# Performance work log

Hardware: AMD Instinct MI355X
Metric: run time of the kernel (lower is better)

The kernel has to match this reference:

```python
import jax, jax.numpy as jnp
import numpy as np
import math

S, B, H, NH = 2048, 1, 4096, 32
D = H // NH  # 128 head dim


def rotate_half(x):
    x1, x2 = x[..., : x.shape[-1] // 2], x[..., x.shape[-1] // 2 :]
    return jnp.concatenate((-x2, x1), axis=-1)


def setup_inputs() -> dict:
    key = jax.random.key(0)
    k1, k2, k3, k4, k5 = jax.random.split(key, 5)
    hidden_states = jax.random.normal(k1, (S, B, H), dtype=jnp.float32)
    position_ids = jnp.broadcast_to(jnp.arange(S, dtype=jnp.int32)[None, :], (B, S))
    # causal mask: True = masked (upper triangle above diagonal)
    attention_mask = jnp.triu(jnp.ones((S, S), dtype=bool), k=1)[None, None]
    W_qkv = jax.random.normal(k2, (H, 3 * H), dtype=jnp.float32) * 0.02
    b_qkv = jax.random.normal(k3, (3 * H,), dtype=jnp.float32) * 0.02
    W_dense = jax.random.normal(k4, (H, H), dtype=jnp.float32) * 0.02
    b_dense = jax.random.normal(k5, (H,), dtype=jnp.float32) * 0.02
    return {
        "hidden_states": hidden_states,
        "position_ids": position_ids,
        "attention_mask": attention_mask,
        "W_qkv": W_qkv,
        "b_qkv": b_qkv,
        "W_dense": W_dense,
        "b_dense": b_dense,
        "layer_id": 27,
    }


def reference(hidden_states, position_ids, attention_mask, W_qkv, b_qkv, W_dense, b_dense, layer_id):
    s, b, h = hidden_states.shape
    nh, d = NH, D
    # QKV projection: [s, b, 3h] -> [s, b, nh, 3d] -> split
    mixed = hidden_states @ W_qkv + b_qkv
    mixed = mixed.reshape(s, b, nh, 3 * d)
    q, k, v = jnp.split(mixed, 3, axis=-1)  # each [s, b, nh, d]
    # rotary embedding indexed by position_ids (transposed to [s, b])
    pos = position_ids.T  # [s, b]
    inv_freq = 1.0 / (10000.0 ** (jnp.arange(0, d, 2, dtype=jnp.float32) / d))
    freqs = pos[..., None].astype(jnp.float32) * inv_freq  # [s, b, d/2]
    emb = jnp.concatenate((freqs, freqs), axis=-1)  # [s, b, d]
    cos = jnp.cos(emb)[:, :, None, :]  # [s, b, 1, d]
    sin = jnp.sin(emb)[:, :, None, :]
    q = q * cos + rotate_half(q) * sin
    k = k * cos + rotate_half(k) * sin
    # attention with per-layer scaling coeff (cancels in softmax except mask fill)
    coeff = jnp.float32(layer_id + 1)
    q_scaled = q / (math.sqrt(d) * coeff)
    scores = jnp.einsum("sbnd,tbnd->bnst", q_scaled, k)  # [b, nh, s, s]
    scores = jnp.where(attention_mask, jnp.float32(-10000.0), scores) * coeff
    probs = jax.nn.softmax(scores, axis=-1)
    ctx = jnp.einsum("bnst,tbnd->sbnd", probs, v).reshape(s, b, h)
    out = ctx @ W_dense + b_dense
    return out
```

## Files before the change

kernel.cpp:

```cpp
#include <hip/hip_runtime.h>

#define S_LEN 2048
#define HID   4096
#define NHEAD 32
#define DHEAD 128
#define H3    12288

typedef __attribute__((ext_vector_type(8))) __bf16 bf16x8;
typedef __attribute__((ext_vector_type(4))) __bf16 bf16x4;
typedef __attribute__((ext_vector_type(4))) float  f32x4;

__device__ __forceinline__ void gl_lds16(const void* g, void* l) {
  __builtin_amdgcn_global_load_lds(
      (const __attribute__((address_space(1))) void*)g,
      (__attribute__((address_space(3))) void*)l, 16, 0, 0);
}

__global__ void cvt_f32_bf16(const float* __restrict__ in, __bf16* __restrict__ out, int n4) {
  int i = blockIdx.x * blockDim.x + threadIdx.x;
  if (i >= n4) return;
  float4 v = ((const float4*)in)[i];
  bf16x4 o;
  o.x = (__bf16)v.x; o.y = (__bf16)v.y; o.z = (__bf16)v.z; o.w = (__bf16)v.w;
  ((bf16x4*)out)[i] = o;
}

__global__ void transpose_cvt(const float* __restrict__ in, __bf16* __restrict__ out, int R, int C) {
  __shared__ float t[64][65];
  const int tid = threadIdx.x;
  const int r0 = blockIdx.y * 64, c0 = blockIdx.x * 64;
#pragma unroll
  for (int p = 0; p < 4; ++p) {
    int r = p * 16 + (tid >> 4);
    int c4 = (tid & 15) * 4;
    float4 v = *(const float4*)(in + (size_t)(r0 + r) * C + c0 + c4);
    t[r][c4] = v.x; t[r][c4 + 1] = v.y; t[r][c4 + 2] = v.z; t[r][c4 + 3] = v.w;
  }
  __syncthreads();
#pragma unroll
  for (int p = 0; p < 4; ++p) {
    int c = p * 16 + (tid >> 4);
    int rg = (tid & 15) * 4;
    bf16x4 o;
    o.x = (__bf16)t[rg][c]; o.y = (__bf16)t[rg + 1][c];
    o.z = (__bf16)t[rg + 2][c]; o.w = (__bf16)t[rg + 3][c];
    *(bf16x4*)(out + (size_t)(c0 + c) * R + r0 + rg) = o;
  }
}

__global__ void rope_kernel(__bf16* __restrict__ q, __bf16* __restrict__ k,
                            const int* __restrict__ pos) {
  int idx = blockIdx.x * 256 + threadIdx.x;
  int j = idx & 63;
  int hs = idx >> 6;
  int s = hs & (S_LEN - 1);
  float p = (float)pos[s];
  float invf = __expf(-(float)j * (9.210340371976184f / 64.f));
  float a = p * invf;
  float c, sn;
  __sincosf(a, &sn, &c);
  const float SC = 0.08838834764831845f;
  size_t base = (size_t)hs * 128;
  float x1 = (float)q[base + j], x2 = (float)q[base + j + 64];
  q[base + j]      = (__bf16)((x1 * c - x2 * sn) * SC);
  q[base + j + 64] = (__bf16)((x2 * c + x1 * sn) * SC);
  x1 = (float)k[base + j]; x2 = (float)k[base + j + 64];
  k[base + j]      = (__bf16)(x1 * c - x2 * sn);
  k[base + j + 64] = (__bf16)(x2 * c + x1 * sn);
}

template <int EPI>
__global__ __launch_bounds__(256, 2)
void gemm_db(const __bf16* __restrict__ A, const __bf16* __restrict__ BT,
             const float* __restrict__ bias, int K,
             __bf16* __restrict__ outq, __bf16* __restrict__ outk,
             __bf16* __restrict__ outvt, float* __restrict__ outf) {
  const int tid = threadIdx.x;
  const int lane = tid & 63;
  const int wave = tid >> 6;
  const int nwg = gridDim.x;
  const int q8 = nwg >> 3;
  const int flat = blockIdx.x;
  const int swz = (flat & 7) * q8 + (flat >> 3);
  const int bm = (swz & 15) * 128;
  const int bn = (swz >> 4) * 128;

  __shared__ char lds[2][32768];

  f32x4 acc[4][4] = {};

  const int wm = (wave >> 1) * 64;
  const int wn = (wave & 1) * 64;

  const int sr = tid >> 3;
  const int sc = (tid & 7) * 16;
  const int scs = sc ^ ((sr & 7) << 4);

  const char* Arow = (const char*)(A + (size_t)(bm + sr) * K) + scs;
  const char* Brow = (const char*)(BT + (size_t)(bn + sr) * K) + scs;

  const int NT = K >> 6;

  auto stage = [&](int t) {
    const char* a_src = Arow + (size_t)t * 128;
    const char* b_src = Brow + (size_t)t * 128;
    char* a_dst = lds[t & 1] + wave * 1024;
    char* b_dst = lds[t & 1] + 16384 + wave * 1024;
#pragma unroll
    for (int i = 0; i < 4; ++i) {
      gl_lds16(a_src + (size_t)i * 32 * K * 2, a_dst + i * 4096);
      gl_lds16(b_src + (size_t)i * 32 * K * 2, b_dst + i * 4096);
    }
  };

  stage(0);
  __syncthreads();
  for (int t = 0; t < NT; ++t) {
    if (t + 1 < NT) stage(t + 1);
    const char* Ab = lds[t & 1];
    const char* Bb = lds[t & 1] + 16384;
#pragma unroll
    for (int kk = 0; kk < 2; ++kk) {
      bf16x8 af[4], bfr[4];
#pragma unroll
      for (int m = 0; m < 4; ++m) {
        int row = wm + m * 16 + (lane & 15);
        int cb = (kk * 64 + ((lane >> 4) << 4)) ^ ((row & 7) << 4);
        af[m] = *(const bf16x8*)(Ab + row * 128 + cb);
      }
#pragma unroll
      for (int n = 0; n < 4; ++n) {
        int row = wn + n * 16 + (lane & 15);
        int cb = (kk * 64 + ((lane >> 4) << 4)) ^ ((row & 7) << 4);
        bfr[n] = *(const bf16x8*)(Bb + row * 128 + cb);
      }
#pragma unroll
      for (int m = 0; m < 4; ++m)
#pragma unroll
        for (int n = 0; n < 4; ++n)
          acc[m][n] = __builtin_amdgcn_mfma_f32_16x16x32_bf16(af[m], bfr[n], acc[m][n], 0, 0, 0);
    }
    __syncthreads();
  }

  const int rbase = (lane >> 4) << 2;
  const int cl = lane & 15;
  if (EPI == 0) {
    const int route = (bn >> 7) % 3;
    const int head = bn / 384;
#pragma unroll
    for (int n = 0; n < 4; ++n) {
      const int d = wn + n * 16 + cl;
      const float bv = bias[bn + d];
#pragma unroll
      for (int m = 0; m < 4; ++m) {
        const int srow = bm + wm + m * 16 + rbase;
        if (route == 2) {
          bf16x4 o;
          o.x = (__bf16)(acc[m][n][0] + bv);
          o.y = (__bf16)(acc[m][n][1] + bv);
          o.z = (__bf16)(acc[m][n][2] + bv);
          o.w = (__bf16)(acc[m][n][3] + bv);
          *(bf16x4*)(outvt + ((size_t)head * 128 + d) * S_LEN + srow) = o;
        } else {
          __bf16* dst = (route == 0 ? outq : outk) + (size_t)head * S_LEN * 128;
#pragma unroll
          for (int r = 0; r < 4; ++r)
            dst[(size_t)(srow + r) * 128 + d] = (__bf16)(acc[m][n][r] + bv);
        }
      }
    }
  } else {
#pragma unroll
    for (int n = 0; n < 4; ++n) {
      const int col = bn + wn + n * 16 + cl;
      const float bv = bias[col];
#pragma unroll
      for (int m = 0; m < 4; ++m) {
        const int srow = bm + wm + m * 16 + rbase;
#pragma unroll
        for (int r = 0; r < 4; ++r)
          outf[(size_t)(srow + r) * HID + col] = acc[m][n][r] + bv;
      }
    }
  }
}

#define ATTN_PROCESS(QF, OACC, MROW, LROW, QT)                                  \
  {                                                                             \
    f32x4 sacc[4] = {};                                                         \
    _Pragma("unroll")                                                           \
    for (int kk = 0; kk < 4; ++kk) {                                            \
      bf16x8 bk[4];                                                             \
      _Pragma("unroll")                                                         \
      for (int n = 0; n < 4; ++n) {                                             \
        int row = n * 16 + cl;                                                  \
        int cb = (kk * 64 + ((lane >> 4) << 4)) ^ ((row & 7) << 4);             \
        bk[n] = *(const bf16x8*)(Kb + row * 256 + cb);                          \
      }                                                                         \
      _Pragma("unroll")                                                         \
      for (int n = 0; n < 4; ++n)                                               \
        sacc[n] = __builtin_amdgcn_mfma_f32_16x16x32_bf16(QF[kk], bk[n], sacc[n], 0, 0, 0); \
    }                                                                           \
    float pmax[4];                                                              \
    _Pragma("unroll")                                                           \
    for (int r = 0; r < 4; ++r) pmax[r] = -1e30f;                               \
    if (j == (QT)) {                                                            \
      _Pragma("unroll")                                                         \
      for (int n = 0; n < 4; ++n) {                                             \
        const int col = n * 16 + cl;                                            \
        _Pragma("unroll")                                                       \
        for (int r = 0; r < 4; ++r) {                                           \
          const int row = wave * 16 + rbase + r;                                \
          float sv = (col > row) ? -1e30f : sacc[n][r];                         \
          sacc[n][r] = sv;                                                      \
          pmax[r] = fmaxf(pmax[r], sv);                                         \
        }                                                                       \
      }                                                                         \
    } else {                                                                    \
      _Pragma("unroll")                                                         \
      for (int n = 0; n < 4; ++n)                                               \
        _Pragma("unroll")                                                       \
        for (int r = 0; r < 4; ++r)                                             \
          pmax[r] = fmaxf(pmax[r], sacc[n][r]);                                 \
    }                                                                           \
    _Pragma("unroll")                                                           \
    for (int xm = 1; xm < 16; xm <<= 1)                                         \
      _Pragma("unroll")                                                         \
      for (int r = 0; r < 4; ++r)                                               \
        pmax[r] = fmaxf(pmax[r], __shfl_xor(pmax[r], xm, 64));                  \
    const bool okd = (pmax[0] <= MROW[0] + 8.f) && (pmax[1] <= MROW[1] + 8.f) && \
                     (pmax[2] <= MROW[2] + 8.f) && (pmax[3] <= MROW[3] + 8.f);  \
    if (__all(okd)) {                                                           \
      _Pragma("unroll")                                                         \
      for (int r = 0; r < 4; ++r) {                                             \
        float psum = 0.f;                                                       \
        _Pragma("unroll")                                                       \
        for (int n = 0; n < 4; ++n) {                                           \
          float pe = __expf(sacc[n][r] - MROW[r]);                              \
          sacc[n][r] = pe;                                                      \
          psum += pe;                                                           \
        }                                                                       \
        _Pragma("unroll")                                                       \
        for (int xm = 1; xm < 16; xm <<= 1)                                     \
          psum += __shfl_xor(psum, xm, 64);                                     \
        LROW[r] += psum;                                                        \
      }                                                                         \
    } else {                                                                    \
      _Pragma("unroll")                                                         \
      for (int r = 0; r < 4; ++r) {                                             \
        const float mnew = fmaxf(MROW[r], pmax[r]);                             \
        const float alpha = __expf(MROW[r] - mnew);                             \
        MROW[r] = mnew;                                                         \
        float psum = 0.f;                                                       \
        _Pragma("unroll")                                                       \
        for (int n = 0; n < 4; ++n) {                                           \
          float pe = __expf(sacc[n][r] - mnew);                                 \
          sacc[n][r] = pe;                                                      \
          psum += pe;                                                           \
        }                                                                       \
        _Pragma("unroll")                                                       \
        for (int xm = 1; xm < 16; xm <<= 1)                                     \
          psum += __shfl_xor(psum, xm, 64);                                     \
        LROW[r] = LROW[r] * alpha + psum;                                       \
        _Pragma("unroll")                                                       \
        for (int nd = 0; nd < 8; ++nd)                                          \
          OACC[nd][r] *= alpha;                                                 \
      }                                                                         \
    }                                                                           \
    _Pragma("unroll")                                                           \
    for (int n = 0; n < 4; ++n) {                                               \
      const int colb = (n * 16 + cl) * 2;                                       \
      _Pragma("unroll")                                                         \
      for (int r = 0; r < 4; ++r) {                                             \
        const int row = rbase + r;                                              \
        *(__bf16*)(Pb + row * 128 + (colb ^ ((row & 7) << 4))) = (__bf16)sacc[n][r]; \
      }                                                                         \
    }                                                                           \
    _Pragma("unroll")                                                           \
    for (int kk = 0; kk < 2; ++kk) {                                            \
      bf16x8 pa, bv[8];                                                         \
      {                                                                         \
        int row = cl;                                                           \
        int cb = (kk * 64 + ((lane >> 4) << 4)) ^ ((row & 7) << 4);             \
        pa = *(const bf16x8*)(Pb + row * 128 + cb);                             \
      }                                                                         \
      _Pragma("unroll")                                                         \
      for (int nd = 0; nd < 8; ++nd) {                                          \
        int row = nd * 16 + cl;                                                 \
        int cb = (kk * 64 + ((lane >> 4) << 4)) ^ ((row & 7) << 4);             \
        bv[nd] = *(const bf16x8*)(Vb + row * 128 + cb);                         \
      }                                                                         \
      _Pragma("unroll")                                                         \
      for (int nd = 0; nd < 8; ++nd)                                            \
        OACC[nd] = __builtin_amdgcn_mfma_f32_16x16x32_bf16(pa, bv[nd], OACC[nd], 0, 0, 0); \
    }                                                                           \
  }

__global__ __launch_bounds__(256, 2)
void attn_kernel(const __bf16* __restrict__ q, const __bf16* __restrict__ k,
                 const __bf16* __restrict__ vt, __bf16* __restrict__ ctx) {
  const int flat = blockIdx.x;
  const int swz = (flat & 7) * 64 + (flat >> 3);
  const int p = swz & 15;
  const int h = swz >> 4;
  const int tid = threadIdx.x, lane = tid & 63, wave = tid >> 6;
  __shared__ char Kd[2][16384];
  __shared__ char Vd[2][16384];
  __shared__ __bf16 Ps[4][16 * 64];
  char* Pb = (char*)(Ps[wave]);

  const __bf16* qh = q + (size_t)h * S_LEN * 128;
  const __bf16* kh = k + (size_t)h * S_LEN * 128;
  const __bf16* vh = vt + (size_t)h * 128 * S_LEN;

  const int cl = lane & 15, rbase = (lane >> 4) << 2;

  const int krow = tid >> 4, kcol = (tid & 15) * 16;
  const int kcs = kcol ^ ((krow & 7) << 4);
  const int vrow = tid >> 3, vcol = (tid & 7) * 16;
  const int vcs = vcol ^ ((vrow & 7) << 4);

  auto stage_kv = [&](int j) {
    {
      const char* src = (const char*)(kh + (size_t)(j * 64 + krow) * 128) + kcs;
      char* dst = Kd[j & 1] + wave * 1024;
#pragma unroll
      for (int i = 0; i < 4; ++i)
        gl_lds16(src + (size_t)i * 16 * 256, dst + i * 4096);
    }
    {
      const char* src = (const char*)(vh + (size_t)vrow * S_LEN + j * 64) + vcs;
      char* dst = Vd[j & 1] + wave * 1024;
#pragma unroll
      for (int i = 0; i < 4; ++i)
        gl_lds16(src + (size_t)i * 32 * (S_LEN * 2), dst + i * 4096);
    }
  };

  const int qtA = p, qtB = 31 - p;

  bf16x8 qfA[4], qfB[4];
  {
    const int rA = qtA * 64 + wave * 16 + cl;
    const int rB = qtB * 64 + wave * 16 + cl;
#pragma unroll
    for (int kk = 0; kk < 4; ++kk) {
      qfA[kk] = *(const bf16x8*)(qh + (size_t)rA * 128 + kk * 32 + ((lane >> 4) << 3));
      qfB[kk] = *(const bf16x8*)(qh + (size_t)rB * 128 + kk * 32 + ((lane >> 4) << 3));
    }
  }

  f32x4 oA[8] = {}, oB[8] = {};
  float mA[4], lA[4], mB[4], lB[4];
#pragma unroll
  for (int r = 0; r < 4; ++r) { mA[r] = -1e30f; lA[r] = 0.f; mB[r] = -1e30f; lB[r] = 0.f; }

  stage_kv(0);
  __syncthreads();
  for (int j = 0; j <= qtB; ++j) {
    if (j < qtB) stage_kv(j + 1);
    const char* Kb = Kd[j & 1];
    const char* Vb = Vd[j & 1];
    ATTN_PROCESS(qfB, oB, mB, lB, qtB)
    if (j <= qtA) ATTN_PROCESS(qfA, oA, mA, lA, qtA)
    __syncthreads();
  }

#pragma unroll
  for (int nd = 0; nd < 8; ++nd) {
    const int d = nd * 16 + cl;
#pragma unroll
    for (int r = 0; r < 4; ++r) {
      const int srowA = qtA * 64 + wave * 16 + rbase + r;
      const int srowB = qtB * 64 + wave * 16 + rbase + r;
      ctx[(size_t)srowA * HID + h * 128 + d] = (__bf16)(oA[nd][r] / lA[r]);
      ctx[(size_t)srowB * HID + h * 128 + d] = (__bf16)(oB[nd][r] / lB[r]);
    }
  }
}

extern "C" void kernel_launch(void* const* d_in, const int* in_sizes, int n_in,
                              void* d_out, int out_size, void* d_ws, size_t ws_size,
                              hipStream_t stream) {
  const float* hs = (const float*)d_in[0];
  const int* pos = (const int*)d_in[1];
  const float* wqkv = (const float*)d_in[3];
  const float* bqkv = (const float*)d_in[4];
  const float* wd = (const float*)d_in[5];
  const float* bd = (const float*)d_in[6];
  float* out = (float*)d_out;

  char* ws = (char*)d_ws;
  const size_t MB = 1024ull * 1024ull;
  if (ws_size < 160 * MB) return;
  __bf16* wT  = (__bf16*)(ws);
  __bf16* xb  = (__bf16*)(ws + 96 * MB);
  __bf16* qb_ = (__bf16*)(ws + 112 * MB);
  __bf16* kb_ = (__bf16*)(ws + 128 * MB);
  __bf16* vtb = (__bf16*)(ws + 144 * MB);

  cvt_f32_bf16<<<8192, 256, 0, stream>>>(hs, xb, 2097152);
  transpose_cvt<<<dim3(192, 64), 256, 0, stream>>>(wqkv, wT, 4096, 12288);
  gemm_db<0><<<1536, 256, 0, stream>>>(xb, wT, bqkv, 4096, qb_, kb_, vtb, nullptr);
  rope_kernel<<<16384, 256, 0, stream>>>(qb_, kb_, pos);
  transpose_cvt<<<dim3(64, 64), 256, 0, stream>>>(wd, wT, 4096, 4096);
  attn_kernel<<<512, 256, 0, stream>>>(qb_, kb_, vtb, xb);
  gemm_db<1><<<512, 256, 0, stream>>>(xb, wT, bd, 4096, nullptr, nullptr, nullptr, out);
}
```

Before: 457.4 us.

## Add 8-wave triple-buffered QKV GEMM with split-K staging and MFMA priority hints

```diff
diff --git a/kernel.cpp b/kernel.cpp
--- a/kernel.cpp
+++ b/kernel.cpp
@@ -69,19 +69,15 @@
   k[base + j + 64] = (__bf16)(x2 * c + x1 * sn);
 }
 
-template <int EPI>
 __global__ __launch_bounds__(256, 2)
-void gemm_db(const __bf16* __restrict__ A, const __bf16* __restrict__ BT,
-             const float* __restrict__ bias, int K,
-             __bf16* __restrict__ outq, __bf16* __restrict__ outk,
-             __bf16* __restrict__ outvt, float* __restrict__ outf) {
+void gemm_dense(const __bf16* __restrict__ A, const __bf16* __restrict__ BT,
+                const float* __restrict__ bias, int K,
+                float* __restrict__ outf) {
   const int tid = threadIdx.x;
   const int lane = tid & 63;
   const int wave = tid >> 6;
-  const int nwg = gridDim.x;
-  const int q8 = nwg >> 3;
   const int flat = blockIdx.x;
-  const int swz = (flat & 7) * q8 + (flat >> 3);
+  const int swz = (flat & 7) * 64 + (flat >> 3);
   const int bm = (swz & 15) * 128;
   const int bn = (swz >> 4) * 128;
 
@@ -145,42 +141,145 @@
 
   const int rbase = (lane >> 4) << 2;
   const int cl = lane & 15;
-  if (EPI == 0) {
-    const int route = (bn >> 7) % 3;
-    const int head = bn / 384;
-#pragma unroll
-    for (int n = 0; n < 4; ++n) {
-      const int d = wn + n * 16 + cl;
-      const float bv = bias[bn + d];
+#pragma unroll
+  for (int n = 0; n < 4; ++n) {
+    const int col = bn + wn + n * 16 + cl;
+    const float bv = bias[col];
+#pragma unroll
+    for (int m = 0; m < 4; ++m) {
+      const int srow = bm + wm + m * 16 + rbase;
+#pragma unroll
+      for (int r = 0; r < 4; ++r)
+        outf[(size_t)(srow + r) * HID + col] = acc[m][n][r] + bv;
+    }
+  }
+}
+
+__global__ __launch_bounds__(512, 2)
+void gemm8p(const __bf16* __restrict__ A, const __bf16* __restrict__ BT,
+            const float* __restrict__ bias, int K,
+            __bf16* __restrict__ outq, __bf16* __restrict__ outk,
+            __bf16* __restrict__ outvt) {
+  const int tid = threadIdx.x, lane = tid & 63, wave = tid >> 6;
+  const int flat = blockIdx.x;
+  const int swz = (flat & 7) * 96 + (flat >> 3);
+  const int bm = (swz & 7) * 256;
+  const int bn = (swz >> 3) * 128;
+
+  __shared__ char lds[3 * 49152];
+
+  const int widM = wave >> 1, widN = wave & 1;
+  const int cl = lane & 15;
+  const int hi16 = (lane >> 4) << 4;
+  const int rbase = (lane >> 4) << 2;
+
+  const int K2 = K * 2;
+  const int sr = tid >> 3;
+  const int scs = ((tid & 7) * 16) ^ ((sr & 7) << 4);
+  const char* Asrc = (const char*)A + (size_t)(bm + sr) * K2 + scs;
+  const char* Bsrc = (const char*)BT + (size_t)(bn + sr) * K2 + scs;
+
+  f32x4 acc[4][4] = {};
+  const int NT = K >> 6;
+
+  auto stageA = [&](int t) {
+    char* d = lds + (t % 3) * 49152 + wave * 1024;
+    const char* s = Asrc + (size_t)t * 128;
+#pragma unroll
+    for (int i = 0; i < 4; ++i)
+      gl_lds16(s + (size_t)(i * 64) * K2, d + i * 8192);
+  };
+  auto stageB = [&](int t) {
+    char* d = lds + (t % 3) * 49152 + 32768 + wave * 1024;
+    const char* s = Bsrc + (size_t)t * 128;
+#pragma unroll
+    for (int i = 0; i < 2; ++i)
+      gl_lds16(s + (size_t)(i * 64) * K2, d + i * 8192);
+  };
+
+  stageA(0); stageB(0); stageA(1); stageB(1);
+  asm volatile("s_waitcnt vmcnt(6)" ::: "memory");
+  asm volatile("s_barrier" ::: "memory");
+
+  for (int t = 0; t < NT; ++t) {
+    const char* sA = lds + (t % 3) * 49152;
+    const char* sB = sA + 32768;
+    {
+      bf16x8 af[4], bfr[4];
 #pragma unroll
       for (int m = 0; m < 4; ++m) {
-        const int srow = bm + wm + m * 16 + rbase;
-        if (route == 2) {
-          bf16x4 o;
-          o.x = (__bf16)(acc[m][n][0] + bv);
-          o.y = (__bf16)(acc[m][n][1] + bv);
-          o.z = (__bf16)(acc[m][n][2] + bv);
-          o.w = (__bf16)(acc[m][n][3] + bv);
-          *(bf16x4*)(outvt + ((size_t)head * 128 + d) * S_LEN + srow) = o;
-        } else {
-          __bf16* dst = (route == 0 ? outq : outk) + (size_t)head * S_LEN * 128;
-#pragma unroll
-          for (int r = 0; r < 4; ++r)
-            dst[(size_t)(srow + r) * 128 + d] = (__bf16)(acc[m][n][r] + bv);
-        }
-      }
-    }
-  } else {
-#pragma unroll
-    for (int n = 0; n < 4; ++n) {
-      const int col = bn + wn + n * 16 + cl;
-      const float bv = bias[col];
+        const int row = widM * 64 + m * 16 + cl;
+        af[m] = *(const bf16x8*)(sA + row * 128 + (hi16 ^ ((row & 7) << 4)));
+      }
+#pragma unroll
+      for (int n = 0; n < 4; ++n) {
+        const int row = widN * 64 + n * 16 + cl;
+        bfr[n] = *(const bf16x8*)(sB + row * 128 + (hi16 ^ ((row & 7) << 4)));
+      }
+      if (t + 2 < NT) stageA(t + 2);
+      asm volatile("s_barrier" ::: "memory");
+      asm volatile("s_waitcnt lgkmcnt(0)" ::: "memory");
+      __builtin_amdgcn_s_setprio(1);
+#pragma unroll
+      for (int m = 0; m < 4; ++m)
+#pragma unroll
+        for (int n = 0; n < 4; ++n)
+          acc[m][n] = __builtin_amdgcn_mfma_f32_16x16x32_bf16(af[m], bfr[n], acc[m][n], 0, 0, 0);
+      __builtin_amdgcn_s_setprio(0);
+      asm volatile("s_barrier" ::: "memory");
+    }
+    {
+      bf16x8 af[4], bfr[4];
 #pragma unroll
       for (int m = 0; m < 4; ++m) {
-        const int srow = bm + wm + m * 16 + rbase;
+        const int row = widM * 64 + m * 16 + cl;
+        af[m] = *(const bf16x8*)(sA + row * 128 + ((64 + hi16) ^ ((row & 7) << 4)));
+      }
+#pragma unroll
+      for (int n = 0; n < 4; ++n) {
+        const int row = widN * 64 + n * 16 + cl;
+        bfr[n] = *(const bf16x8*)(sB + row * 128 + ((64 + hi16) ^ ((row & 7) << 4)));
+      }
+      if (t + 2 < NT) {
+        stageB(t + 2);
+        asm volatile("s_waitcnt vmcnt(6)" ::: "memory");
+      } else {
+        asm volatile("s_waitcnt vmcnt(0)" ::: "memory");
+      }
+      asm volatile("s_barrier" ::: "memory");
+      asm volatile("s_waitcnt lgkmcnt(0)" ::: "memory");
+      __builtin_amdgcn_s_setprio(1);
+#pragma unroll
+      for (int m = 0; m < 4; ++m)
+#pragma unroll
+        for (int n = 0; n < 4; ++n)
+          acc[m][n] = __builtin_amdgcn_mfma_f32_16x16x32_bf16(af[m], bfr[n], acc[m][n], 0, 0, 0);
+      __builtin_amdgcn_s_setprio(0);
+      asm volatile("s_barrier" ::: "memory");
+    }
+  }
+
+  const int route = (bn >> 7) % 3;
+  const int head = bn / 384;
+#pragma unroll
+  for (int n = 0; n < 4; ++n) {
+    const int d = widN * 64 + n * 16 + cl;
+    const float bv = bias[bn + d];
+#pragma unroll
+    for (int m = 0; m < 4; ++m) {
+      const int srow = bm + widM * 64 + m * 16 + rbase;
+      if (route == 2) {
+        bf16x4 o;
+        o.x = (__bf16)(acc[m][n][0] + bv);
+        o.y = (__bf16)(acc[m][n][1] + bv);
+        o.z = (__bf16)(acc[m][n][2] + bv);
+        o.w = (__bf16)(acc[m][n][3] + bv);
+        *(bf16x4*)(outvt + ((size_t)head * 128 + d) * S_LEN + srow) = o;
+      } else {
+        __bf16* dst = (route == 0 ? outq : outk) + (size_t)head * S_LEN * 128;
 #pragma unroll
         for (int r = 0; r < 4; ++r)
-          outf[(size_t)(srow + r) * HID + col] = acc[m][n][r] + bv;
+          dst[(size_t)(srow + r) * 128 + d] = (__bf16)(acc[m][n][r] + bv);
       }
     }
   }
@@ -198,9 +297,11 @@
         int cb = (kk * 64 + ((lane >> 4) << 4)) ^ ((row & 7) << 4);             \
         bk[n] = *(const bf16x8*)(Kb + row * 256 + cb);                          \
       }                                                                         \
+      __builtin_amdgcn_s_setprio(1);                                            \
       _Pragma("unroll")                                                         \
       for (int n = 0; n < 4; ++n)                                               \
         sacc[n] = __builtin_amdgcn_mfma_f32_16x16x32_bf16(QF[kk], bk[n], sacc[n], 0, 0, 0); \
+      __builtin_amdgcn_s_setprio(0);                                            \
     }                                                                           \
     float pmax[4];                                                              \
     _Pragma("unroll")                                                           \
@@ -291,9 +392,11 @@
         int cb = (kk * 64 + ((lane >> 4) << 4)) ^ ((row & 7) << 4);             \
         bv[nd] = *(const bf16x8*)(Vb + row * 128 + cb);                         \
       }                                                                         \
+      __builtin_amdgcn_s_setprio(1);                                            \
       _Pragma("unroll")                                                         \
       for (int nd = 0; nd < 8; ++nd)                                            \
         OACC[nd] = __builtin_amdgcn_mfma_f32_16x16x32_bf16(pa, bv[nd], OACC[nd], 0, 0, 0); \
+      __builtin_amdgcn_s_setprio(0);                                            \
     }                                                                           \
   }
 
@@ -402,9 +505,9 @@
 
   cvt_f32_bf16<<<8192, 256, 0, stream>>>(hs, xb, 2097152);
   transpose_cvt<<<dim3(192, 64), 256, 0, stream>>>(wqkv, wT, 4096, 12288);
-  gemm_db<0><<<1536, 256, 0, stream>>>(xb, wT, bqkv, 4096, qb_, kb_, vtb, nullptr);
+  gemm8p<<<768, 512, 0, stream>>>(xb, wT, bqkv, 4096, qb_, kb_, vtb);
   rope_kernel<<<16384, 256, 0, stream>>>(qb_, kb_, pos);
   transpose_cvt<<<dim3(64, 64), 256, 0, stream>>>(wd, wT, 4096, 4096);
   attn_kernel<<<512, 256, 0, stream>>>(qb_, kb_, vtb, xb);
-  gemm_db<1><<<512, 256, 0, stream>>>(xb, wT, bd, 4096, nullptr, nullptr, nullptr, out);
-}
+  gemm_dense<<<512, 256, 0, stream>>>(xb, wT, bd, 4096, out);
+}
```

After: 471.2 us. 1.03x slower.
